# Optimization experiments

Hardware: AMD Instinct MI355X
Metric: run time of the kernel (lower is better)

## Reference

```python
import jax, jax.numpy as jnp
import numpy as np

N, C, T, V, K = 1024, 32, 8, 64, 3
CT = C * T  # = in_channels = out_channels of the 1x1 convs


def setup_inputs() -> dict:
    key = jax.random.key(0)
    k1, k2, k3, k4 = jax.random.split(key, 4)
    x = jax.random.normal(k1, (N, C, T, V), dtype=jnp.float32)
    # stacked per-branch 1x1-conv weights (Conv2d(CT, CT, 1) == Linear over CT)
    W = jax.random.normal(k2, (K, CT, CT), dtype=jnp.float32) * (1.0 / np.sqrt(CT))
    b = jax.random.normal(k3, (K, CT), dtype=jnp.float32) * 0.01
    # learnable adjacency stack A: (K, V, V)
    A = jax.random.normal(k4, (K, V, V), dtype=jnp.float32) * 0.1
    return {"x": x, "W": W, "b": b, "A": A}


def reference(x, W, b, A):
    n, c, t, v = x.shape
    ct = c * t
    # (N,C,T,V) -> (N,V,C*T): each node's feature vector over channels*time
    xf = x.transpose(0, 3, 1, 2).reshape(n, v, ct)
    # per-branch 1x1 conv == per-branch linear over CT: (K,N,V,CT)
    y = jnp.einsum('nvc,kdc->knvd', xf, W) + b[:, None, None, :]
    # adjacency aggregation per branch, summed over branches (replaces cat+sum)
    out = jnp.einsum('knvd,kvw->nwd', y, A)  # (N,V,CT)
    # (N,V,C,T) -> (N,C,V,T), matching y.sum(-1).permute(0,1,3,2)
    return out.reshape(n, v, c, t).transpose(0, 2, 1, 3)
```

## Files before the change

### kernel.cpp

```cpp
#include <hip/hip_runtime.h>


typedef __attribute__((ext_vector_type(8))) short bf16x8;
typedef __attribute__((ext_vector_type(4))) float f32x4;

__device__ __forceinline__ short f2bf(float f) {
  union { float f; unsigned u; } c; c.f = f;
  unsigned r = c.u + 0x7FFFu + ((c.u >> 16) & 1u);
  return (short)(r >> 16);
}

#define ASW_OFF  393216
#define BIAS_OFF 417792

__global__ __launch_bounds__(256) void prep_kernel(
    const float* __restrict__ W, const float* __restrict__ b,
    const float* __restrict__ A, short* __restrict__ Wsw,
    short* __restrict__ Asw, float* __restrict__ bias2T) {
  int t = blockIdx.x * 256 + threadIdx.x;
  if (t < 196608) {
    int e = t & 7, l = (t >> 3) & 63, ks = (t >> 9) & 7, mt = (t >> 12) & 3,
        wv = (t >> 14) & 3, k = t >> 16;
    int d = wv * 64 + mt * 16 + (l & 15);
    int c = ks * 32 + (l >> 4) * 8 + e;
    Wsw[t] = f2bf(W[(k * 256 + d) * 256 + c]);
  } else if (t < 196608 + 12288) {
    int t2 = t - 196608;
    int e = t2 & 7, l = (t2 >> 3) & 63, nt = (t2 >> 9) & 3, ks = (t2 >> 11) & 1,
        k = t2 >> 12;
    int w = nt * 16 + (l & 15);
    int v = ks * 32 + (l >> 4) * 8 + e;
    Asw[t2] = f2bf(A[(k * 64 + v) * 64 + w]);
  } else {
    int t2 = t - 196608 - 12288;
    int d = t2 >> 6, w = t2 & 63;
    float s = 0.f;
    for (int k = 0; k < 3; ++k) {
      float cs = 0.f;
      for (int v = 0; v < 64; ++v) cs += A[(k * 64 + v) * 64 + w];
      s += cs * b[k * 256 + d];
    }
    bias2T[t2] = s;
  }
}

#define UT_STRIDE 264

__global__ __launch_bounds__(256, 2) void gcn_main(
    const float* __restrict__ x, const short* __restrict__ Wsw,
    const short* __restrict__ Asw, const float* __restrict__ bias2T,
    float* __restrict__ out) {
  __shared__ short Ut[64 * UT_STRIDE];

  const int tid = threadIdx.x;
  const int wv = tid >> 6;
  const int lane = tid & 63;
  const int li = lane & 15;
  const int lq = lane >> 4;
  const int n = blockIdx.x;

  const float* xn = x + (size_t)n * 16384;

  bf16x8 xf[2][4];
#pragma unroll
  for (int ks = 0; ks < 2; ++ks)
#pragma unroll
    for (int mt = 0; mt < 4; ++mt) {
      int row = 64 * wv + mt * 16 + li;
      int v0 = ks * 32 + lq * 8;
      const float4* p = (const float4*)(xn + row * 64 + v0);
      float4 f0 = p[0], f1 = p[1];
      bf16x8 tt;
      tt[0] = f2bf(f0.x); tt[1] = f2bf(f0.y); tt[2] = f2bf(f0.z); tt[3] = f2bf(f0.w);
      tt[4] = f2bf(f1.x); tt[5] = f2bf(f1.y); tt[6] = f2bf(f1.z); tt[7] = f2bf(f1.w);
      xf[ks][mt] = tt;
    }

  f32x4 acc2[4][4];
#pragma unroll
  for (int mt = 0; mt < 4; ++mt)
#pragma unroll
    for (int nt = 0; nt < 4; ++nt)
      acc2[mt][nt] = (f32x4){0.f, 0.f, 0.f, 0.f};

  for (int k = 0; k < 3; ++k) {
    f32x4 acc1[4][4];
#pragma unroll
    for (int mt = 0; mt < 4; ++mt)
#pragma unroll
      for (int nt = 0; nt < 4; ++nt)
        acc1[mt][nt] = (f32x4){0.f, 0.f, 0.f, 0.f};

    const short* AswK = Asw + k * 4096;
#pragma unroll
    for (int ks = 0; ks < 2; ++ks) {
      bf16x8 bfr[4];
#pragma unroll
      for (int nt = 0; nt < 4; ++nt)
        bfr[nt] = *(const bf16x8*)(AswK + ((ks * 4 + nt) * 64 + lane) * 8);
#pragma unroll
      for (int mt = 0; mt < 4; ++mt)
#pragma unroll
        for (int nt = 0; nt < 4; ++nt)
          acc1[mt][nt] = __builtin_amdgcn_mfma_f32_16x16x32_bf16(
              xf[ks][mt], bfr[nt], acc1[mt][nt], 0, 0, 0);
    }

    __syncthreads();

#pragma unroll
    for (int mt = 0; mt < 4; ++mt)
#pragma unroll
      for (int nt = 0; nt < 4; ++nt) {
        int w = nt * 16 + li;
        int ct = 64 * wv + mt * 16 + 4 * lq;
        union { short s[4]; unsigned long long u; } p;
        p.s[0] = f2bf(acc1[mt][nt][0]);
        p.s[1] = f2bf(acc1[mt][nt][1]);
        p.s[2] = f2bf(acc1[mt][nt][2]);
        p.s[3] = f2bf(acc1[mt][nt][3]);
        *(unsigned long long*)(&Ut[w * UT_STRIDE + ct]) = p.u;
      }

    __syncthreads();

    const short* WswK = Wsw + (k * 4 + wv) * 16384;
#pragma unroll
    for (int ks = 0; ks < 8; ++ks) {
      bf16x8 aw[4], bu[4];
#pragma unroll
      for (int mt = 0; mt < 4; ++mt)
        aw[mt] = *(const bf16x8*)(WswK + ((mt * 8 + ks) * 64 + lane) * 8);
#pragma unroll
      for (int nt = 0; nt < 4; ++nt)
        bu[nt] = *(const bf16x8*)(&Ut[(nt * 16 + li) * UT_STRIDE + ks * 32 + lq * 8]);
#pragma unroll
      for (int mt = 0; mt < 4; ++mt)
#pragma unroll
        for (int nt = 0; nt < 4; ++nt)
          acc2[mt][nt] = __builtin_amdgcn_mfma_f32_16x16x32_bf16(
              aw[mt], bu[nt], acc2[mt][nt], 0, 0, 0);
    }
  }

  __syncthreads();

  float* ep = ((float*)Ut) + wv * 2112;
  float* outn = out + (size_t)n * 16384 + wv * 4096;

#pragma unroll
  for (int pass = 0; pass < 2; ++pass) {
#pragma unroll
    for (int mth = 0; mth < 2; ++mth) {
      int mt = pass * 2 + mth;
#pragma unroll
      for (int nt = 0; nt < 4; ++nt) {
        int w = nt * 16 + li;
#pragma unroll
        for (int r = 0; r < 4; ++r) {
          int dl = mt * 16 + 4 * lq + r;
          int dl2 = dl - pass * 32;
          ep[dl2 * 65 + w] =
              acc2[mt][nt][r] + bias2T[(64 * wv + dl) * 64 + w];
        }
      }
    }
#pragma unroll
    for (int it = 0; it < 8; ++it) {
      int jj2 = it * 256 + lane * 4;
      int cl2 = jj2 >> 9;
      int w = (jj2 >> 3) & 63;
      int t0 = jj2 & 7;
      float4 vv;
      vv.x = ep[(cl2 * 8 + t0 + 0) * 65 + w];
      vv.y = ep[(cl2 * 8 + t0 + 1) * 65 + w];
      vv.z = ep[(cl2 * 8 + t0 + 2) * 65 + w];
      vv.w = ep[(cl2 * 8 + t0 + 3) * 65 + w];
      *(float4*)(outn + pass * 2048 + jj2) = vv;
    }
  }
}

extern "C" void kernel_launch(void* const* d_in, const int* in_sizes, int n_in,
                              void* d_out, int out_size, void* d_ws, size_t ws_size,
                              hipStream_t stream) {
  (void)in_sizes; (void)n_in; (void)out_size; (void)ws_size;
  const float* x = (const float*)d_in[0];
  const float* W = (const float*)d_in[1];
  const float* b = (const float*)d_in[2];
  const float* A = (const float*)d_in[3];
  float* out = (float*)d_out;

  short* Wsw = (short*)d_ws;
  short* Asw = (short*)((char*)d_ws + ASW_OFF);
  float* bias2T = (float*)((char*)d_ws + BIAS_OFF);

  prep_kernel<<<880, 256, 0, stream>>>(W, b, A, Wsw, Asw, bias2T);
  gcn_main<<<1024, 256, 0, stream>>>(x, Wsw, Asw, bias2T, out);
}
```

Before: 153.8 us.

## Fold bias into accumulator init, store output directly, and split stage-1 accumulators

The precomputed bias is transposed to a column-major layout and used to initialise the second-stage accumulators, so the bias add in the epilogue goes away. The LDS-staged transpose epilogue is replaced by direct float4 global stores. Stage-1 accumulators are split into two halves, the k loop is fully unrolled, and launch bounds ask for three blocks per CU to cut register pressure and raise occupancy. It also uses packed bf16 conversion intrinsics and removes one barrier. Risks include register spills at the higher occupancy target and less coalesced direct stores.

Measured after the change: 210.2 us. 1.37x slower.

```diff
diff --git a/kernel.cpp b/kernel.cpp
--- a/kernel.cpp
+++ b/kernel.cpp
@@ -1,4 +1,5 @@
 #include <hip/hip_runtime.h>
+#include <hip/hip_bf16.h>
 
 
 typedef __attribute__((ext_vector_type(8))) short bf16x8;
@@ -10,13 +11,20 @@
   return (short)(r >> 16);
 }
 
+__device__ __forceinline__ unsigned pkbf(float a, float b) {
+  float2 t; t.x = a; t.y = b;
+  union { __hip_bfloat162 h; unsigned u; } c;
+  c.h = __float22bfloat162_rn(t);
+  return c.u;
+}
+
 #define ASW_OFF  393216
 #define BIAS_OFF 417792
 
 __global__ __launch_bounds__(256) void prep_kernel(
     const float* __restrict__ W, const float* __restrict__ b,
     const float* __restrict__ A, short* __restrict__ Wsw,
-    short* __restrict__ Asw, float* __restrict__ bias2T) {
+    short* __restrict__ Asw, float* __restrict__ biasCM) {
   int t = blockIdx.x * 256 + threadIdx.x;
   if (t < 196608) {
     int e = t & 7, l = (t >> 3) & 63, ks = (t >> 9) & 7, mt = (t >> 12) & 3,
@@ -33,22 +41,23 @@
     Asw[t2] = f2bf(A[(k * 64 + v) * 64 + w]);
   } else {
     int t2 = t - 196608 - 12288;
-    int d = t2 >> 6, w = t2 & 63;
+    int w = t2 >> 8, d = t2 & 255;
     float s = 0.f;
     for (int k = 0; k < 3; ++k) {
       float cs = 0.f;
+#pragma unroll
       for (int v = 0; v < 64; ++v) cs += A[(k * 64 + v) * 64 + w];
       s += cs * b[k * 256 + d];
     }
-    bias2T[t2] = s;
+    biasCM[t2] = s;
   }
 }
 
 #define UT_STRIDE 264
 
-__global__ __launch_bounds__(256, 2) void gcn_main(
+__global__ __launch_bounds__(256, 3) void gcn_main(
     const float* __restrict__ x, const short* __restrict__ Wsw,
-    const short* __restrict__ Asw, const float* __restrict__ bias2T,
+    const short* __restrict__ Asw, const float* __restrict__ biasCM,
     float* __restrict__ out) {
   __shared__ short Ut[64 * UT_STRIDE];
 
@@ -60,67 +69,71 @@
   const int n = blockIdx.x;
 
   const float* xn = x + (size_t)n * 16384;
+  float* outn = out + (size_t)n * 16384;
+
+  f32x4 acc2[4][4];
+#pragma unroll
+  for (int mt = 0; mt < 4; ++mt)
+#pragma unroll
+    for (int nt = 0; nt < 4; ++nt) {
+      const float4 bb = *(const float4*)(biasCM + (nt * 16 + li) * 256 +
+                                         64 * wv + mt * 16 + 4 * lq);
+      acc2[mt][nt] = (f32x4){bb.x, bb.y, bb.z, bb.w};
+    }
 
   bf16x8 xf[2][4];
 #pragma unroll
   for (int ks = 0; ks < 2; ++ks)
 #pragma unroll
     for (int mt = 0; mt < 4; ++mt) {
-      int row = 64 * wv + mt * 16 + li;
-      int v0 = ks * 32 + lq * 8;
-      const float4* p = (const float4*)(xn + row * 64 + v0);
+      const float4* p =
+          (const float4*)(xn + (64 * wv + mt * 16 + li) * 64 + ks * 32 + lq * 8);
       float4 f0 = p[0], f1 = p[1];
-      bf16x8 tt;
-      tt[0] = f2bf(f0.x); tt[1] = f2bf(f0.y); tt[2] = f2bf(f0.z); tt[3] = f2bf(f0.w);
-      tt[4] = f2bf(f1.x); tt[5] = f2bf(f1.y); tt[6] = f2bf(f1.z); tt[7] = f2bf(f1.w);
-      xf[ks][mt] = tt;
+      union { bf16x8 v; unsigned u[4]; } t;
+      t.u[0] = pkbf(f0.x, f0.y); t.u[1] = pkbf(f0.z, f0.w);
+      t.u[2] = pkbf(f1.x, f1.y); t.u[3] = pkbf(f1.z, f1.w);
+      xf[ks][mt] = t.v;
     }
 
-  f32x4 acc2[4][4];
 #pragma unroll
-  for (int mt = 0; mt < 4; ++mt)
+  for (int k = 0; k < 3; ++k) {
+    const short* AswK = Asw + k * 4096;
+
 #pragma unroll
-    for (int nt = 0; nt < 4; ++nt)
-      acc2[mt][nt] = (f32x4){0.f, 0.f, 0.f, 0.f};
-
-  for (int k = 0; k < 3; ++k) {
-    f32x4 acc1[4][4];
+    for (int h = 0; h < 2; ++h) {
+      f32x4 acc1[2][4];
 #pragma unroll
-    for (int mt = 0; mt < 4; ++mt)
-#pragma unroll
-      for (int nt = 0; nt < 4; ++nt)
-        acc1[mt][nt] = (f32x4){0.f, 0.f, 0.f, 0.f};
-
-    const short* AswK = Asw + k * 4096;
-#pragma unroll
-    for (int ks = 0; ks < 2; ++ks) {
-      bf16x8 bfr[4];
-#pragma unroll
-      for (int nt = 0; nt < 4; ++nt)
-        bfr[nt] = *(const bf16x8*)(AswK + ((ks * 4 + nt) * 64 + lane) * 8);
-#pragma unroll
-      for (int mt = 0; mt < 4; ++mt)
+      for (int m2 = 0; m2 < 2; ++m2)
 #pragma unroll
         for (int nt = 0; nt < 4; ++nt)
-          acc1[mt][nt] = __builtin_amdgcn_mfma_f32_16x16x32_bf16(
-              xf[ks][mt], bfr[nt], acc1[mt][nt], 0, 0, 0);
-    }
-
-    __syncthreads();
+          acc1[m2][nt] = (f32x4){0.f, 0.f, 0.f, 0.f};
 
 #pragma unroll
-    for (int mt = 0; mt < 4; ++mt)
+      for (int ks = 0; ks < 2; ++ks) {
+        bf16x8 bfr[4];
 #pragma unroll
-      for (int nt = 0; nt < 4; ++nt) {
-        int w = nt * 16 + li;
-        int ct = 64 * wv + mt * 16 + 4 * lq;
-        union { short s[4]; unsigned long long u; } p;
-        p.s[0] = f2bf(acc1[mt][nt][0]);
-        p.s[1] = f2bf(acc1[mt][nt][1]);
-        p.s[2] = f2bf(acc1[mt][nt][2]);
-        p.s[3] = f2bf(acc1[mt][nt][3]);
-        *(unsigned long long*)(&Ut[w * UT_STRIDE + ct]) = p.u;
+        for (int nt = 0; nt < 4; ++nt)
+          bfr[nt] = *(const bf16x8*)(AswK + ((ks * 4 + nt) * 64 + lane) * 8);
+#pragma unroll
+        for (int m2 = 0; m2 < 2; ++m2)
+#pragma unroll
+          for (int nt = 0; nt < 4; ++nt)
+            acc1[m2][nt] = __builtin_amdgcn_mfma_f32_16x16x32_bf16(
+                xf[ks][2 * h + m2], bfr[nt], acc1[m2][nt], 0, 0, 0);
       }
+
+#pragma unroll
+      for (int m2 = 0; m2 < 2; ++m2)
+#pragma unroll
+        for (int nt = 0; nt < 4; ++nt) {
+          int w = nt * 16 + li;
+          int ct = 64 * wv + (2 * h + m2) * 16 + 4 * lq;
+          union { unsigned u[2]; unsigned long long ull; } p;
+          p.u[0] = pkbf(acc1[m2][nt][0], acc1[m2][nt][1]);
+          p.u[1] = pkbf(acc1[m2][nt][2], acc1[m2][nt][3]);
+          *(unsigned long long*)(&Ut[w * UT_STRIDE + ct]) = p.ull;
+        }
+    }
 
     __syncthreads();
 
@@ -141,44 +154,22 @@
           acc2[mt][nt] = __builtin_amdgcn_mfma_f32_16x16x32_bf16(
               aw[mt], bu[nt], acc2[mt][nt], 0, 0, 0);
     }
+
+    if (k < 2) __syncthreads();
   }
 
-  __syncthreads();
-
-  float* ep = ((float*)Ut) + wv * 2112;
-  float* outn = out + (size_t)n * 16384 + wv * 4096;
-
 #pragma unroll
-  for (int pass = 0; pass < 2; ++pass) {
+  for (int mt = 0; mt < 4; ++mt)
 #pragma unroll
-    for (int mth = 0; mth < 2; ++mth) {
-      int mt = pass * 2 + mth;
-#pragma unroll
-      for (int nt = 0; nt < 4; ++nt) {
-        int w = nt * 16 + li;
-#pragma unroll
-        for (int r = 0; r < 4; ++r) {
-          int dl = mt * 16 + 4 * lq + r;
-          int dl2 = dl - pass * 32;
-          ep[dl2 * 65 + w] =
-              acc2[mt][nt][r] + bias2T[(64 * wv + dl) * 64 + w];
-        }
-      }
+    for (int nt = 0; nt < 4; ++nt) {
+      float4 vv;
+      vv.x = acc2[mt][nt][0];
+      vv.y = acc2[mt][nt][1];
+      vv.z = acc2[mt][nt][2];
+      vv.w = acc2[mt][nt][3];
+      *(float4*)(outn + (8 * wv + 2 * mt + (lq >> 1)) * 512 +
+                 (nt * 16 + li) * 8 + 4 * (lq & 1)) = vv;
     }
-#pragma unroll
-    for (int it = 0; it < 8; ++it) {
-      int jj2 = it * 256 + lane * 4;
-      int cl2 = jj2 >> 9;
-      int w = (jj2 >> 3) & 63;
-      int t0 = jj2 & 7;
-      float4 vv;
-      vv.x = ep[(cl2 * 8 + t0 + 0) * 65 + w];
-      vv.y = ep[(cl2 * 8 + t0 + 1) * 65 + w];
-      vv.z = ep[(cl2 * 8 + t0 + 2) * 65 + w];
-      vv.w = ep[(cl2 * 8 + t0 + 3) * 65 + w];
-      *(float4*)(outn + pass * 2048 + jj2) = vv;
-    }
-  }
 }
 
 extern "C" void kernel_launch(void* const* d_in, const int* in_sizes, int n_in,
@@ -193,8 +184,8 @@
 
   short* Wsw = (short*)d_ws;
   short* Asw = (short*)((char*)d_ws + ASW_OFF);
-  float* bias2T = (float*)((char*)d_ws + BIAS_OFF);
+  float* biasCM = (float*)((char*)d_ws + BIAS_OFF);
 
-  prep_kernel<<<880, 256, 0, stream>>>(W, b, A, Wsw, Asw, bias2T);
-  gcn_main<<<1024, 256, 0, stream>>>(x, Wsw, Asw, bias2T, out);
+  prep_kernel<<<880, 256, 0, stream>>>(W, b, A, Wsw, Asw, biasCM);
+  gcn_main<<<1024, 256, 0, stream>>>(x, Wsw, Asw, biasCM, out);
 }
```
